# Kernel tuning notes

Measured on AMD Instinct MI355X. Metric: run time of the kernel, lower is better.

## Reference

```python
import jax, jax.numpy as jnp
import numpy as np

N_NODES = 50000
N_EDGES = 400000
D = 256
EDGE_DIM = 64
N_LAYERS = 3


def setup_inputs() -> dict:
    key = jax.random.key(0)
    ks = jax.random.split(key, 8)
    sc = 1.0 / np.sqrt(D)
    x = jax.random.normal(ks[0], (N_NODES, D), dtype=jnp.float32)
    edge_attr = jax.random.normal(ks[1], (N_EDGES, EDGE_DIM), dtype=jnp.float32)
    edge_index = jax.random.randint(ks[2], (2, N_EDGES), 0, N_NODES, dtype=jnp.int64)
    Wl = jax.random.normal(ks[3], (N_LAYERS, D, D), dtype=jnp.float32) * sc
    bl = jax.random.normal(ks[4], (N_LAYERS, D), dtype=jnp.float32) * 0.01
    Wr = jax.random.normal(ks[5], (N_LAYERS, D, D), dtype=jnp.float32) * sc
    We = jax.random.normal(ks[6], (N_LAYERS, D, EDGE_DIM), dtype=jnp.float32) * (1.0 / np.sqrt(EDGE_DIM))
    be = jax.random.normal(ks[7], (N_LAYERS, D), dtype=jnp.float32) * 0.01
    return {"x": x, "edge_attr": edge_attr, "edge_index": edge_index,
            "Wl": Wl, "bl": bl, "Wr": Wr, "We": We, "be": be}


def reference(x, edge_attr, edge_index, Wl, bl, Wr, We, be):
    # SAGEConv (mean aggr, root_weight=True, no normalize) with edge-feature
    # augmented messages: msg = x[src] + edge_lin(edge_attr)
    src, dst = edge_index[0], edge_index[1]
    n = x.shape[0]
    # per-target in-degree for mean aggregation (computed once; edge_index fixed)
    deg = jax.ops.segment_sum(jnp.ones((edge_index.shape[1],), x.dtype), dst,
                              num_segments=n)
    inv_deg = (1.0 / jnp.maximum(deg, 1.0))[:, None]  # [N,1]
    for l in range(Wl.shape[0]):
        e_msg = edge_attr @ We[l].T + be[l]                 # [E,D] edge_lin
        msg = x[src] + e_msg                                 # gather + add
        agg = jax.ops.segment_sum(msg, dst, num_segments=n) * inv_deg  # mean
        x = jax.nn.relu(agg @ Wl[l].T + bl[l] + x @ Wr[l].T)
    return x
```

## Files before the change

### kernel.cpp

```cpp
#include <hip/hip_runtime.h>

typedef __attribute__((ext_vector_type(8))) short bf16x8;
typedef __attribute__((ext_vector_type(4))) float f32x4;
typedef unsigned short u16;

__device__ __forceinline__ u16 f2bf(float f) {
    union { float f; unsigned u; } v; v.f = f;
    unsigned u = v.u;
    return (u16)((u + 0x7FFFu + ((u >> 16) & 1u)) >> 16);
}
__device__ __forceinline__ float bf2f(u16 h) {
    union { unsigned u; float f; } v; v.u = ((unsigned)h) << 16;
    return v.f;
}

__global__ __launch_bounds__(256) void k_convert(const float* __restrict__ x,
                                                 u16* __restrict__ hb, int total4) {
    int i = blockIdx.x * 256 + threadIdx.x;
    if (i >= total4) return;
    float4 v = ((const float4*)x)[i];
    ushort4 o;
    o.x = f2bf(v.x); o.y = f2bf(v.y); o.z = f2bf(v.z); o.w = f2bf(v.w);
    ((ushort4*)hb)[i] = o;
}

__global__ __launch_bounds__(256) void k_count(const int* __restrict__ dst,
                                               int* __restrict__ deg, int E) {
    int e = blockIdx.x * 256 + threadIdx.x;
    if (e < E) atomicAdd(&deg[dst[e]], 1);
}

__global__ __launch_bounds__(256) void k_part(const int* __restrict__ deg,
                                              int* __restrict__ part, int N) {
    __shared__ int ws[4];
    int i = blockIdx.x * 256 + threadIdx.x;
    int v = (i < N) ? deg[i] : 0;
#pragma unroll
    for (int o = 32; o; o >>= 1) v += __shfl_down(v, o);
    int lane = threadIdx.x & 63, w = threadIdx.x >> 6;
    if (lane == 0) ws[w] = v;
    __syncthreads();
    if (threadIdx.x == 0) part[blockIdx.x] = ws[0] + ws[1] + ws[2] + ws[3];
}

__global__ __launch_bounds__(256) void k_scanp(const int* __restrict__ part,
                                               int* __restrict__ bases, int P) {
    __shared__ int s[256];
    int t = threadIdx.x;
    int v = (t < P) ? part[t] : 0;
    s[t] = v;
    __syncthreads();
#pragma unroll
    for (int o = 1; o < 256; o <<= 1) {
        int u = (t >= o) ? s[t - o] : 0;
        __syncthreads();
        s[t] += u;
        __syncthreads();
    }
    bases[t] = s[t] - v;
}

__global__ __launch_bounds__(256) void k_apply(const int* __restrict__ deg,
                                               const int* __restrict__ bases,
                                               int* __restrict__ rp, int* __restrict__ cur,
                                               int N, int E) {
    __shared__ int s[256];
    int b = blockIdx.x, t = threadIdx.x;
    int i = b * 256 + t;
    int d = (i < N) ? deg[i] : 0;
    s[t] = d;
    __syncthreads();
#pragma unroll
    for (int o = 1; o < 256; o <<= 1) {
        int u = (t >= o) ? s[t - o] : 0;
        __syncthreads();
        s[t] += u;
        __syncthreads();
    }
    if (i < N) {
        int r = bases[b] + s[t] - d;
        rp[i] = r;
        cur[i] = r;
    }
    if (b == (int)gridDim.x - 1 && t == 255) rp[N] = E;
}

__global__ __launch_bounds__(256) void k_fill(const int* __restrict__ dst, const int* __restrict__ src,
                                              int* __restrict__ cur,
                                              int* __restrict__ eid, int* __restrict__ srcs, int E) {
    int e = blockIdx.x * 256 + threadIdx.x;
    if (e < E) {
        int p = atomicAdd(&cur[dst[e]], 1);
        eid[p] = e;
        srcs[p] = src[e];
    }
}

__global__ __launch_bounds__(256) void k_sa(const float* __restrict__ attr, const int* __restrict__ rp,
                                            const int* __restrict__ eid, u16* __restrict__ Sa,
                                            unsigned char* __restrict__ hasdeg, int N) {
    int v = blockIdx.x * 4 + (threadIdx.x >> 6);
    if (v >= N) return;
    int l = threadIdx.x & 63;
    int g = l >> 4;
    int c = (l & 15) * 4;
    int j0 = rp[v], j1 = rp[v + 1];
    float4 a = {0.f, 0.f, 0.f, 0.f};
    int j = j0;
    for (; j + 7 < j1; j += 8) {
        int e0 = eid[j + g];
        int e1 = eid[j + 4 + g];
        float4 x0 = *(const float4*)&attr[(size_t)e0 * 64 + c];
        float4 x1 = *(const float4*)&attr[(size_t)e1 * 64 + c];
        a.x += x0.x + x1.x; a.y += x0.y + x1.y;
        a.z += x0.z + x1.z; a.w += x0.w + x1.w;
    }
    for (; j < j1; j += 4) {
        int jj = j + g;
        if (jj < j1) {
            int e = eid[jj];
            float4 x0 = *(const float4*)&attr[(size_t)e * 64 + c];
            a.x += x0.x; a.y += x0.y; a.z += x0.z; a.w += x0.w;
        }
    }
    a.x += __shfl_xor(a.x, 16); a.y += __shfl_xor(a.y, 16);
    a.z += __shfl_xor(a.z, 16); a.w += __shfl_xor(a.w, 16);
    a.x += __shfl_xor(a.x, 32); a.y += __shfl_xor(a.y, 32);
    a.z += __shfl_xor(a.z, 32); a.w += __shfl_xor(a.w, 32);
    int dg = j1 - j0;
    float m = 1.f / (float)(dg > 1 ? dg : 1);
    if (l < 16) {
        ushort4 o;
        o.x = f2bf(a.x * m); o.y = f2bf(a.y * m);
        o.z = f2bf(a.z * m); o.w = f2bf(a.w * m);
        *(ushort4*)&Sa[(size_t)v * 64 + c] = o;
        if (l == 0) hasdeg[v] = (dg > 0) ? 1 : 0;
    }
}

__global__ __launch_bounds__(256) void k_sx(const u16* __restrict__ hb, const int* __restrict__ rp,
                                            const int* __restrict__ srcs,
                                            u16* __restrict__ Sx, int N) {
    int v = blockIdx.x * 4 + (threadIdx.x >> 6);
    if (v >= N) return;
    int l = threadIdx.x & 63;
    int h = l >> 5;
    int c = (l & 31) * 8;
    int j0 = rp[v], j1 = rp[v + 1];
    float a[8] = {0.f, 0.f, 0.f, 0.f, 0.f, 0.f, 0.f, 0.f};
    int j = j0;
    for (; j + 3 < j1; j += 4) {
        int s0 = srcs[j + h];
        int s1 = srcs[j + 2 + h];
        bf16x8 u0 = *(const bf16x8*)&hb[(size_t)s0 * 256 + c];
        bf16x8 u1 = *(const bf16x8*)&hb[(size_t)s1 * 256 + c];
#pragma unroll
        for (int i = 0; i < 8; ++i) a[i] += bf2f((u16)u0[i]) + bf2f((u16)u1[i]);
    }
    for (; j < j1; j += 2) {
        int jj = j + h;
        if (jj < j1) {
            int s0 = srcs[jj];
            bf16x8 u0 = *(const bf16x8*)&hb[(size_t)s0 * 256 + c];
#pragma unroll
            for (int i = 0; i < 8; ++i) a[i] += bf2f((u16)u0[i]);
        }
    }
#pragma unroll
    for (int i = 0; i < 8; ++i) a[i] += __shfl_xor(a[i], 32);
    int dg = j1 - j0;
    float m = 1.f / (float)(dg > 1 ? dg : 1);
    if (l < 32) {
        bf16x8 o;
#pragma unroll
        for (int i = 0; i < 8; ++i) o[i] = (short)f2bf(a[i] * m);
        *(bf16x8*)&Sx[(size_t)v * 256 + c] = o;
    }
}

__global__ __launch_bounds__(256) void k_wprep(const float* __restrict__ Wl, const float* __restrict__ Wr,
                                               const float* __restrict__ We, const float* __restrict__ be,
                                               u16* __restrict__ Wlb, u16* __restrict__ Wrb,
                                               u16* __restrict__ Wleb, float* __restrict__ wlbe) {
    int t = blockIdx.x * 256 + threadIdx.x;
    if (t < 3 * 65536) { Wlb[t] = f2bf(Wl[t]); Wrb[t] = f2bf(Wr[t]); }
    if (t < 3 * 16384) {
        int l = t >> 14;
        int r = t & 16383;
        int d = r >> 6, jj = r & 63;
        const float* wl = Wl + ((size_t)l << 16) + (size_t)d * 256;
        const float* we = We + ((size_t)l << 14) + jj;
        float s = 0.f;
        for (int p = 0; p < 256; ++p) s += wl[p] * we[(size_t)p * 64];
        Wleb[t] = f2bf(s);
    }
    if (t < 768) {
        int l = t >> 8, d = t & 255;
        const float* wl = Wl + ((size_t)l << 16) + (size_t)d * 256;
        const float* b = be + l * 256;
        float s = 0.f;
        for (int p = 0; p < 256; ++p) s += wl[p] * b[p];
        wlbe[t] = s;
    }
}

__device__ __forceinline__ void do_seg(const u16* __restrict__ A, const u16* __restrict__ B,
                                       int lda, int K, int r0, int c0, int M,
                                       u16* Alds, u16* Blds,
                                       int lane, int w, int wr, int wc,
                                       int r16, int kq, f32x4 (&acc)[4][4]) {
    const int rloc = lane >> 3;
    const int cE = (lane & 7) * 8;
    for (int k0 = 0; k0 < K; k0 += 64) {
        __syncthreads();
#pragma unroll
        for (int i = 0; i < 4; ++i) {
            int ch = w * 4 + i;
            int ar = r0 + ch * 8 + rloc;
            ar = ar < M ? ar : M - 1;
            __builtin_amdgcn_global_load_lds(
                (const __attribute__((address_space(1))) void*)(A + (size_t)ar * lda + k0 + cE),
                (__attribute__((address_space(3))) void*)(Alds + ch * 512), 16, 0, 0);
            int br = c0 + ch * 8 + rloc;
            __builtin_amdgcn_global_load_lds(
                (const __attribute__((address_space(1))) void*)(B + (size_t)br * K + k0 + cE),
                (__attribute__((address_space(3))) void*)(Blds + ch * 512), 16, 0, 0);
        }
        __syncthreads();
        bf16x8 af[4][2], bfr[4][2];
#pragma unroll
        for (int rf = 0; rf < 4; ++rf) {
            af[rf][0] = *(const bf16x8*)&Alds[(wr * 64 + rf * 16 + r16) * 64 + kq];
            af[rf][1] = *(const bf16x8*)&Alds[(wr * 64 + rf * 16 + r16) * 64 + 32 + kq];
        }
#pragma unroll
        for (int cf = 0; cf < 4; ++cf) {
            bfr[cf][0] = *(const bf16x8*)&Blds[(wc * 64 + cf * 16 + r16) * 64 + kq];
            bfr[cf][1] = *(const bf16x8*)&Blds[(wc * 64 + cf * 16 + r16) * 64 + 32 + kq];
        }
#pragma unroll
        for (int rf = 0; rf < 4; ++rf)
#pragma unroll
            for (int cf = 0; cf < 4; ++cf) {
                acc[rf][cf] = __builtin_amdgcn_mfma_f32_16x16x32_bf16(af[rf][0], bfr[cf][0], acc[rf][cf], 0, 0, 0);
                acc[rf][cf] = __builtin_amdgcn_mfma_f32_16x16x32_bf16(af[rf][1], bfr[cf][1], acc[rf][cf], 0, 0, 0);
            }
    }
}

__global__ __launch_bounds__(256, 4) void k_gemm(
    const u16* __restrict__ Sx, const u16* __restrict__ Hb, const u16* __restrict__ Sa,
    const u16* __restrict__ Wlb, const u16* __restrict__ Wrb, const u16* __restrict__ Wleb,
    const float* __restrict__ bl, const float* __restrict__ wlbe,
    const unsigned char* __restrict__ hasdeg,
    u16* hb_out, float* f_out, int M)
{
    __shared__ __align__(16) u16 Alds[128 * 64];
    __shared__ __align__(16) u16 Blds[128 * 64];
    const int tid = threadIdx.x;
    const int lane = tid & 63;
    const int w = tid >> 6;
    const int wr = w & 1, wc = w >> 1;
    const int r16 = lane & 15;
    const int hi = lane >> 4;
    const int kq = hi * 8;
    const int rb = blockIdx.x >> 1;
    const int cb = blockIdx.x & 1;
    const int r0 = rb * 128;
    const int c0 = cb * 128;

    const f32x4 fzero = {0.f, 0.f, 0.f, 0.f};
    f32x4 acc[4][4];
#pragma unroll
    for (int a = 0; a < 4; ++a)
#pragma unroll
        for (int b = 0; b < 4; ++b) acc[a][b] = fzero;

    do_seg(Sx, Wlb, 256, 256, r0, c0, M, Alds, Blds, lane, w, wr, wc, r16, kq, acc);
    do_seg(Hb, Wrb, 256, 256, r0, c0, M, Alds, Blds, lane, w, wr, wc, r16, kq, acc);
    do_seg(Sa, Wleb, 64, 64, r0, c0, M, Alds, Blds, lane, w, wr, wc, r16, kq, acc);

    float blv[4], wbev[4];
#pragma unroll
    for (int cf = 0; cf < 4; ++cf) {
        int col = c0 + wc * 64 + 16 * cf + r16;
        blv[cf] = bl[col];
        wbev[cf] = wlbe[col];
    }
#pragma unroll
    for (int rf = 0; rf < 4; ++rf)
#pragma unroll
        for (int j = 0; j < 4; ++j) {
            int r = r0 + wr * 64 + 16 * rf + 4 * hi + j;
            if (r < M) {
                float hd = hasdeg[r] ? 1.f : 0.f;
#pragma unroll
                for (int cf = 0; cf < 4; ++cf) {
                    int col = c0 + wc * 64 + 16 * cf + r16;
                    float v = acc[rf][cf][j] + blv[cf] + hd * wbev[cf];
                    v = fmaxf(v, 0.f);
                    if (f_out) f_out[(size_t)r * 256 + col] = v;
                    if (hb_out) hb_out[(size_t)r * 256 + col] = f2bf(v);
                }
            }
        }
}

extern "C" void kernel_launch(void* const* d_in, const int* in_sizes, int n_in,
                              void* d_out, int out_size, void* d_ws, size_t ws_size,
                              hipStream_t stream) {
    const float* x    = (const float*)d_in[0];
    const float* attr = (const float*)d_in[1];
    const int*   ei   = (const int*)d_in[2];
    const float* Wl   = (const float*)d_in[3];
    const float* bl   = (const float*)d_in[4];
    const float* Wr   = (const float*)d_in[5];
    const float* We   = (const float*)d_in[6];
    const float* be   = (const float*)d_in[7];
    float* out = (float*)d_out;

    const int N = in_sizes[0] / 256;
    const int E = in_sizes[1] / 64;
    const int* srcA = ei;
    const int* dstA = ei + E;

    char* p = (char*)d_ws;
    auto carve = [&](size_t bytes) -> char* {
        char* q = p;
        p += (bytes + 255) & ~(size_t)255;
        return q;
    };
    u16* hb0    = (u16*)carve((size_t)N * 256 * 2);
    u16* hb1    = (u16*)carve((size_t)N * 256 * 2);
    u16* SxB    = (u16*)carve((size_t)N * 256 * 2);
    u16* SaB    = (u16*)carve((size_t)N * 64 * 2);
    u16* Wlb    = (u16*)carve((size_t)3 * 65536 * 2);
    u16* Wrb    = (u16*)carve((size_t)3 * 65536 * 2);
    u16* Wleb   = (u16*)carve((size_t)3 * 16384 * 2);
    float* wlbe = (float*)carve((size_t)3 * 256 * 4);
    int* deg    = (int*)carve((size_t)N * 4);
    int* rp     = (int*)carve((size_t)(N + 1) * 4);
    int* cur    = (int*)carve((size_t)N * 4);
    int* eid    = (int*)carve((size_t)E * 4);
    int* srcs   = (int*)carve((size_t)E * 4);
    int* part   = (int*)carve((size_t)256 * 4);
    int* bases  = (int*)carve((size_t)256 * 4);
    unsigned char* hasdeg = (unsigned char*)carve((size_t)N);

    hipMemsetAsync(deg, 0, (size_t)N * 4, stream);

    int t4 = N * 64;
    k_convert<<<(t4 + 255) / 256, 256, 0, stream>>>(x, hb0, t4);
    k_count<<<(E + 255) / 256, 256, 0, stream>>>(dstA, deg, E);
    const int PB = (N + 255) / 256;
    k_part<<<PB, 256, 0, stream>>>(deg, part, N);
    k_scanp<<<1, 256, 0, stream>>>(part, bases, PB);
    k_apply<<<PB, 256, 0, stream>>>(deg, bases, rp, cur, N, E);
    k_fill<<<(E + 255) / 256, 256, 0, stream>>>(dstA, srcA, cur, eid, srcs, E);
    k_sa<<<(N + 3) / 4, 256, 0, stream>>>(attr, rp, eid, SaB, hasdeg, N);
    k_wprep<<<(3 * 65536 + 255) / 256, 256, 0, stream>>>(Wl, Wr, We, be, Wlb, Wrb, Wleb, wlbe);

    const int RB = (N + 127) / 128;
    const int gblocks = RB * 2;
    u16* hcur = hb0;
    u16* hnxt = hb1;
    for (int l = 0; l < 3; ++l) {
        k_sx<<<(N + 3) / 4, 256, 0, stream>>>(hcur, rp, srcs, SxB, N);
        k_gemm<<<gblocks, 256, 0, stream>>>(SxB, hcur, SaB,
            Wlb + l * 65536, Wrb + l * 65536, Wleb + l * 16384,
            bl + l * 256, wlbe + l * 256, hasdeg,
            (l < 2) ? hnxt : (u16*)nullptr, (l == 2) ? out : (float*)nullptr, N);
        u16* t = hcur; hcur = hnxt; hnxt = t;
    }
}
```

Measured before the change: 324.0 us.

## Use full-width 64x256 GEMM tiles, update node features in place, unroll gather

The fused SAGE GEMM now uses 64-row by 256-column tiles, so each block covers every output column. Each row of Sx, H and Sa is then loaded once per layer instead of once per column block, which cuts global A-operand traffic. Because a block owns whole rows, the next-layer bf16 features are written in place over the input buffer, and the ping-pong buffer is dropped. The k_sx neighbour gather now processes 8 edges per iteration to keep more loads in flight. The trade-off is a larger LDS footprint for the B tile, a lower occupancy hint (3 blocks instead of 4) and fewer blocks in the grid.

```diff
diff --git a/kernel.cpp b/kernel.cpp
--- a/kernel.cpp
+++ b/kernel.cpp
@@ -149,13 +149,18 @@
     int j0 = rp[v], j1 = rp[v + 1];
     float a[8] = {0.f, 0.f, 0.f, 0.f, 0.f, 0.f, 0.f, 0.f};
     int j = j0;
-    for (; j + 3 < j1; j += 4) {
+    for (; j + 7 < j1; j += 8) {
         int s0 = srcs[j + h];
         int s1 = srcs[j + 2 + h];
+        int s2 = srcs[j + 4 + h];
+        int s3 = srcs[j + 6 + h];
         bf16x8 u0 = *(const bf16x8*)&hb[(size_t)s0 * 256 + c];
         bf16x8 u1 = *(const bf16x8*)&hb[(size_t)s1 * 256 + c];
-#pragma unroll
-        for (int i = 0; i < 8; ++i) a[i] += bf2f((u16)u0[i]) + bf2f((u16)u1[i]);
+        bf16x8 u2 = *(const bf16x8*)&hb[(size_t)s2 * 256 + c];
+        bf16x8 u3 = *(const bf16x8*)&hb[(size_t)s3 * 256 + c];
+#pragma unroll
+        for (int i = 0; i < 8; ++i)
+            a[i] += (bf2f((u16)u0[i]) + bf2f((u16)u1[i])) + (bf2f((u16)u2[i]) + bf2f((u16)u3[i]));
     }
     for (; j < j1; j += 2) {
         int jj = j + h;
@@ -205,38 +210,42 @@
 }
 
 __device__ __forceinline__ void do_seg(const u16* __restrict__ A, const u16* __restrict__ B,
-                                       int lda, int K, int r0, int c0, int M,
+                                       int lda, int K, int r0, int M,
                                        u16* Alds, u16* Blds,
-                                       int lane, int w, int wr, int wc,
+                                       int lane, int w,
                                        int r16, int kq, f32x4 (&acc)[4][4]) {
     const int rloc = lane >> 3;
     const int cE = (lane & 7) * 8;
     for (int k0 = 0; k0 < K; k0 += 64) {
         __syncthreads();
 #pragma unroll
-        for (int i = 0; i < 4; ++i) {
-            int ch = w * 4 + i;
-            int ar = r0 + ch * 8 + rloc;
+        for (int i = 0; i < 2; ++i) {
+            int rowb = i * 32 + w * 8;
+            int ar = r0 + rowb + rloc;
             ar = ar < M ? ar : M - 1;
             __builtin_amdgcn_global_load_lds(
                 (const __attribute__((address_space(1))) void*)(A + (size_t)ar * lda + k0 + cE),
-                (__attribute__((address_space(3))) void*)(Alds + ch * 512), 16, 0, 0);
-            int br = c0 + ch * 8 + rloc;
+                (__attribute__((address_space(3))) void*)(Alds + (size_t)rowb * 64), 16, 0, 0);
+        }
+#pragma unroll
+        for (int i = 0; i < 8; ++i) {
+            int rowb = i * 32 + w * 8;
+            int br = rowb + rloc;
             __builtin_amdgcn_global_load_lds(
                 (const __attribute__((address_space(1))) void*)(B + (size_t)br * K + k0 + cE),
-                (__attribute__((address_space(3))) void*)(Blds + ch * 512), 16, 0, 0);
+                (__attribute__((address_space(3))) void*)(Blds + (size_t)rowb * 64), 16, 0, 0);
         }
         __syncthreads();
         bf16x8 af[4][2], bfr[4][2];
 #pragma unroll
         for (int rf = 0; rf < 4; ++rf) {
-            af[rf][0] = *(const bf16x8*)&Alds[(wr * 64 + rf * 16 + r16) * 64 + kq];
-            af[rf][1] = *(const bf16x8*)&Alds[(wr * 64 + rf * 16 + r16) * 64 + 32 + kq];
+            af[rf][0] = *(const bf16x8*)&Alds[(rf * 16 + r16) * 64 + kq];
+            af[rf][1] = *(const bf16x8*)&Alds[(rf * 16 + r16) * 64 + 32 + kq];
         }
 #pragma unroll
         for (int cf = 0; cf < 4; ++cf) {
-            bfr[cf][0] = *(const bf16x8*)&Blds[(wc * 64 + cf * 16 + r16) * 64 + kq];
-            bfr[cf][1] = *(const bf16x8*)&Blds[(wc * 64 + cf * 16 + r16) * 64 + 32 + kq];
+            bfr[cf][0] = *(const bf16x8*)&Blds[(w * 64 + cf * 16 + r16) * 64 + kq];
+            bfr[cf][1] = *(const bf16x8*)&Blds[(w * 64 + cf * 16 + r16) * 64 + 32 + kq];
         }
 #pragma unroll
         for (int rf = 0; rf < 4; ++rf)
@@ -248,26 +257,22 @@
     }
 }
 
-__global__ __launch_bounds__(256, 4) void k_gemm(
+__global__ __launch_bounds__(256, 3) void k_gemm(
     const u16* __restrict__ Sx, const u16* __restrict__ Hb, const u16* __restrict__ Sa,
     const u16* __restrict__ Wlb, const u16* __restrict__ Wrb, const u16* __restrict__ Wleb,
     const float* __restrict__ bl, const float* __restrict__ wlbe,
     const unsigned char* __restrict__ hasdeg,
     u16* hb_out, float* f_out, int M)
 {
-    __shared__ __align__(16) u16 Alds[128 * 64];
-    __shared__ __align__(16) u16 Blds[128 * 64];
+    __shared__ __align__(16) u16 Alds[64 * 64];
+    __shared__ __align__(16) u16 Blds[256 * 64];
     const int tid = threadIdx.x;
     const int lane = tid & 63;
     const int w = tid >> 6;
-    const int wr = w & 1, wc = w >> 1;
     const int r16 = lane & 15;
     const int hi = lane >> 4;
     const int kq = hi * 8;
-    const int rb = blockIdx.x >> 1;
-    const int cb = blockIdx.x & 1;
-    const int r0 = rb * 128;
-    const int c0 = cb * 128;
+    const int r0 = blockIdx.x * 64;
 
     const f32x4 fzero = {0.f, 0.f, 0.f, 0.f};
     f32x4 acc[4][4];
@@ -276,14 +281,14 @@
 #pragma unroll
         for (int b = 0; b < 4; ++b) acc[a][b] = fzero;
 
-    do_seg(Sx, Wlb, 256, 256, r0, c0, M, Alds, Blds, lane, w, wr, wc, r16, kq, acc);
-    do_seg(Hb, Wrb, 256, 256, r0, c0, M, Alds, Blds, lane, w, wr, wc, r16, kq, acc);
-    do_seg(Sa, Wleb, 64, 64, r0, c0, M, Alds, Blds, lane, w, wr, wc, r16, kq, acc);
+    do_seg(Sx, Wlb, 256, 256, r0, M, Alds, Blds, lane, w, r16, kq, acc);
+    do_seg(Hb, Wrb, 256, 256, r0, M, Alds, Blds, lane, w, r16, kq, acc);
+    do_seg(Sa, Wleb, 64, 64, r0, M, Alds, Blds, lane, w, r16, kq, acc);
 
     float blv[4], wbev[4];
 #pragma unroll
     for (int cf = 0; cf < 4; ++cf) {
-        int col = c0 + wc * 64 + 16 * cf + r16;
+        int col = w * 64 + 16 * cf + r16;
         blv[cf] = bl[col];
         wbev[cf] = wlbe[col];
     }
@@ -291,12 +296,12 @@
     for (int rf = 0; rf < 4; ++rf)
 #pragma unroll
         for (int j = 0; j < 4; ++j) {
-            int r = r0 + wr * 64 + 16 * rf + 4 * hi + j;
+            int r = r0 + 16 * rf + 4 * hi + j;
             if (r < M) {
                 float hd = hasdeg[r] ? 1.f : 0.f;
 #pragma unroll
                 for (int cf = 0; cf < 4; ++cf) {
-                    int col = c0 + wc * 64 + 16 * cf + r16;
+                    int col = w * 64 + 16 * cf + r16;
                     float v = acc[rf][cf][j] + blv[cf] + hd * wbev[cf];
                     v = fmaxf(v, 0.f);
                     if (f_out) f_out[(size_t)r * 256 + col] = v;
@@ -330,8 +335,7 @@
         p += (bytes + 255) & ~(size_t)255;
         return q;
     };
-    u16* hb0    = (u16*)carve((size_t)N * 256 * 2);
-    u16* hb1    = (u16*)carve((size_t)N * 256 * 2);
+    u16* hb     = (u16*)carve((size_t)N * 256 * 2);
     u16* SxB    = (u16*)carve((size_t)N * 256 * 2);
     u16* SaB    = (u16*)carve((size_t)N * 64 * 2);
     u16* Wlb    = (u16*)carve((size_t)3 * 65536 * 2);
@@ -350,7 +354,7 @@
     hipMemsetAsync(deg, 0, (size_t)N * 4, stream);
 
     int t4 = N * 64;
-    k_convert<<<(t4 + 255) / 256, 256, 0, stream>>>(x, hb0, t4);
+    k_convert<<<(t4 + 255) / 256, 256, 0, stream>>>(x, hb, t4);
     k_count<<<(E + 255) / 256, 256, 0, stream>>>(dstA, deg, E);
     const int PB = (N + 255) / 256;
     k_part<<<PB, 256, 0, stream>>>(deg, part, N);
@@ -360,16 +364,12 @@
     k_sa<<<(N + 3) / 4, 256, 0, stream>>>(attr, rp, eid, SaB, hasdeg, N);
     k_wprep<<<(3 * 65536 + 255) / 256, 256, 0, stream>>>(Wl, Wr, We, be, Wlb, Wrb, Wleb, wlbe);
 
-    const int RB = (N + 127) / 128;
-    const int gblocks = RB * 2;
-    u16* hcur = hb0;
-    u16* hnxt = hb1;
+    const int gblocks = (N + 63) / 64;
     for (int l = 0; l < 3; ++l) {
-        k_sx<<<(N + 3) / 4, 256, 0, stream>>>(hcur, rp, srcs, SxB, N);
-        k_gemm<<<gblocks, 256, 0, stream>>>(SxB, hcur, SaB,
+        k_sx<<<(N + 3) / 4, 256, 0, stream>>>(hb, rp, srcs, SxB, N);
+        k_gemm<<<gblocks, 256, 0, stream>>>(SxB, hb, SaB,
             Wlb + l * 65536, Wrb + l * 65536, Wleb + l * 16384,
             bl + l * 256, wlbe + l * 256, hasdeg,
-            (l < 2) ? hnxt : (u16*)nullptr, (l == 2) ? out : (float*)nullptr, N);
-        u16* t = hcur; hcur = hnxt; hnxt = t;
-    }
-}
+            (l < 2) ? hb : (u16*)nullptr, (l == 2) ? out : (float*)nullptr, N);
+    }
+}
```

Result: slower. 332.3 us (+2.6%).
